# Optimization experiments

Hardware: AMD Instinct MI355X
Metric: run time of the kernel (lower is better)

The kernel has to match this reference:

```python
import jax, jax.numpy as jnp
import numpy as np
from jax import lax

NDF = 128
OUT_CH = 256
N_INPUT = 4096
H = W = 64
A_FEAT = OUT_CH * 2 * 2   # 1024
B_OUT = OUT_CH            # 256
C_ROW = 16
BATCH = 128
EPS = 1e-5


def conv2d_s2(x, w):
    # x: NCHW, w: OIHW, stride 2, pad 1 (kernel 4) -> halves spatial dims
    return lax.conv_general_dilated(x, w, window_strides=(2, 2),
                                    padding=[(1, 1), (1, 1)],
                                    dimension_numbers=("NCHW", "OIHW", "NCHW"))


def batchnorm(x, gamma, beta):
    # training-mode batch stats over (N, H, W)
    mean = jnp.mean(x, axis=(0, 2, 3), keepdims=True)
    var = jnp.var(x, axis=(0, 2, 3), keepdims=True)
    xn = (x - mean) * lax.rsqrt(var + EPS)
    return xn * gamma[None, :, None, None] + beta[None, :, None, None]


def lrelu(x):
    return jnp.where(x >= 0, x, 0.2 * x)


def setup_inputs() -> dict:
    key = jax.random.key(0)
    ks = jax.random.split(key, 16)
    s = lambda fan: 1.0 / np.sqrt(fan)
    inp = {
        "image": jax.random.normal(ks[0], (BATCH, 3, H, W), jnp.float32),
        "word_vectors": jax.random.normal(ks[1], (BATCH, N_INPUT), jnp.float32),
        "fc_w": jax.random.normal(ks[2], (H * W, N_INPUT), jnp.float32) * s(N_INPUT),
        "w1": jax.random.normal(ks[3], (NDF, 4, 4, 4), jnp.float32) * s(4 * 16),
        "w2": jax.random.normal(ks[4], (NDF * 2, NDF, 4, 4), jnp.float32) * s(NDF * 16),
        "w3": jax.random.normal(ks[5], (NDF * 2, NDF * 2, 4, 4), jnp.float32) * s(NDF * 2 * 16),
        "w4": jax.random.normal(ks[6], (NDF * 4, NDF * 2, 4, 4), jnp.float32) * s(NDF * 2 * 16),
        "w5": jax.random.normal(ks[7], (OUT_CH, NDF * 4, 4, 4), jnp.float32) * s(NDF * 4 * 16),
        "g2": jnp.ones((NDF * 2,), jnp.float32),
        "b2": jnp.zeros((NDF * 2,), jnp.float32),
        "g3": jnp.ones((NDF * 2,), jnp.float32),
        "b3": jnp.zeros((NDF * 2,), jnp.float32),
        "g4": jnp.ones((NDF * 4,), jnp.float32),
        "b4": jnp.zeros((NDF * 4,), jnp.float32),
        "T": jax.random.uniform(ks[8], (A_FEAT, B_OUT, C_ROW), jnp.float32,
                                 minval=0.0, maxval=1.0 / A_FEAT),
    }
    return inp


def reference(image, word_vectors, fc_w, w1, w2, w3, w4, w5,
              g2, b2, g3, b3, g4, b4, T):
    b = image.shape[0]
    # fc: Linear(no bias) + ReLU (dropout = identity at p=0 / eval)
    wv = jax.nn.relu(word_vectors @ fc_w.T)            # [b, H*W]
    wv = wv.reshape(b, 1, H, W)
    x = jnp.concatenate([image, wv], axis=1)           # [b, 4, 64, 64]
    # conv stack (spectral norm acts on weights; raw weights used here)
    x = lrelu(conv2d_s2(x, w1))                        # [b, ndf, 32, 32]
    x = lrelu(batchnorm(conv2d_s2(x, w2), g2, b2))     # [b, 2ndf, 16, 16]
    x = lrelu(batchnorm(conv2d_s2(x, w3), g3, b3))     # [b, 2ndf, 8, 8]
    x = lrelu(batchnorm(conv2d_s2(x, w4), g4, b4))     # [b, 4ndf, 4, 4]
    x = conv2d_s2(x, w5)                               # [b, out_ch, 2, 2]
    # minibatch discrimination
    feat = x.reshape(b, A_FEAT)                        # [b, 1024]
    Ms = (feat @ T.reshape(A_FEAT, B_OUT * C_ROW)).reshape(b, B_OUT, C_ROW)
    # pairwise L1 over C, exp, sum over batch (including self, as in the loop)
    d = jnp.sum(jnp.abs(Ms[:, None, :, :] - Ms[None, :, :, :]), axis=-1)  # [b,b,B]
    mbd = jnp.sum(jnp.exp(-d), axis=1)                 # [b, B]
    return jnp.concatenate([feat, mbd], axis=1)        # [b, 1280]
```

## Files before the change

kernel.cpp:

```cpp
#include <hip/hip_runtime.h>
#include <cstddef>

#define BB 128

typedef unsigned short u16;
typedef __attribute__((ext_vector_type(8))) short short8;
typedef __attribute__((ext_vector_type(4))) short short4v;
typedef __attribute__((ext_vector_type(4))) float f32x4;

constexpr int ilog2c(int v){ return v<=1 ? 0 : 1+ilog2c(v>>1); }

__device__ __forceinline__ u16 f2b(float f){
  union {float f; unsigned u;} x; x.f = f;
  unsigned u = x.u + 0x7fffu + ((x.u>>16)&1u);
  return (u16)(u>>16);
}
__device__ __forceinline__ float b2f(u16 h){
  union {unsigned u; float f;} x; x.u = ((unsigned)h)<<16;
  return x.f;
}

#define GLOAD_LDS16(gsrc, ldsdst) \
  __builtin_amdgcn_global_load_lds((const __attribute__((address_space(1))) void*)(gsrc), \
      (__attribute__((address_space(3))) void*)(ldsdst), 16, 0, 0)

template<int IC, int OC, int OH, int STORE, int KSPLIT=1>
__global__ __launch_bounds__(512) void convmm2(
    const u16* __restrict__ xp, const u16* __restrict__ wtT, void* __restrict__ yv)
{
  constexpr int OW = OH, S = OH*OW;
  constexpr int IHp = 2*OH+2, IWp = 2*OW+2;
  constexpr int KT = 16*IC;
  constexpr int KTS = KT / KSPLIT;
  constexpr int NT = KTS / 64;
  constexpr int M = BB * S;
  constexpr int LS = ilog2c(S), LOW = ilog2c(OW), L4 = ilog2c(4*IC);
  __shared__ u16 As[2*128*64];
  __shared__ u16 Bs[2*128*64];
  const int tid = threadIdx.x;
  const int n0 = blockIdx.x*128;
  const int m0 = blockIdx.y*128;
  const int kbase = (KSPLIT>1) ? blockIdx.z*KTS : 0;
  const int wave = tid>>6, l = tid&63;
  const int wm = wave>>1, wn = wave&1;

  size_t abase[2]; int au[2];
  #pragma unroll
  for (int t=0;t<2;++t){
    int unit = tid + t*512;
    int r = unit>>3, us = unit&7;
    au[t] = us ^ (r&7);
    int p = m0 + r;
    int b = p >> LS, s = p & (S-1);
    int oh = s >> LOW, ow = s & (OW-1);
    abase[t] = ((size_t)(b*IHp + 2*oh)*IWp + 2*ow)*IC;
  }
  const u16* bsrc[2];
  #pragma unroll
  for (int t=0;t<2;++t){
    int unit = tid + t*512;
    int r = unit>>3, us = unit&7;
    bsrc[t] = wtT + (size_t)(n0+r)*KT + (size_t)(us ^ (r&7))*8;
  }

  auto stage = [&](int half, int k0){
    #pragma unroll
    for (int t=0;t<2;++t){
      int k = k0 + au[t]*8;
      int kh = k >> L4, koff = k & (4*IC-1);
      GLOAD_LDS16(xp + abase[t] + (size_t)kh*IWp*IC + koff,
                  &As[half*8192 + (size_t)(t*512 + wave*64)*8]);
    }
    #pragma unroll
    for (int t=0;t<2;++t){
      GLOAD_LDS16(bsrc[t] + k0, &Bs[half*8192 + (size_t)(t*512 + wave*64)*8]);
    }
  };

  f32x4 acc[2][4] = {};

  stage(0, kbase);
  __syncthreads();
  int cur = 0;
  for (int t=0; t<NT; ++t){
    if (t+1 < NT) stage(cur^1, kbase + (t+1)*64);
    #pragma unroll
    for (int kk=0;kk<2;++kk){
      short8 af[2], bfm[4];
      #pragma unroll
      for (int mi=0;mi<2;++mi){
        int row = wm*32 + mi*16 + (l&15);
        int u = (kk*4 + (l>>4)) ^ (row&7);
        af[mi] = *(const short8*)(&As[cur*8192 + row*64 + u*8]);
      }
      #pragma unroll
      for (int ni=0;ni<4;++ni){
        int row = wn*64 + ni*16 + (l&15);
        int u = (kk*4 + (l>>4)) ^ (row&7);
        bfm[ni] = *(const short8*)(&Bs[cur*8192 + row*64 + u*8]);
      }
      #pragma unroll
      for (int mi=0;mi<2;++mi)
        #pragma unroll
        for (int ni=0;ni<4;++ni)
          acc[mi][ni] = __builtin_amdgcn_mfma_f32_16x16x32_bf16(af[mi], bfm[ni], acc[mi][ni], 0,0,0);
    }
    __syncthreads();
    cur ^= 1;
  }
  #pragma unroll
  for (int mi=0;mi<2;++mi){
    #pragma unroll
    for (int ni=0;ni<4;++ni){
      #pragma unroll
      for (int r=0;r<4;++r){
        int row = m0 + wm*32 + mi*16 + (l>>4)*4 + r;
        int col = n0 + wn*64 + ni*16 + (l&15);
        float v = acc[mi][ni][r];
        if (STORE==0){
          ((u16*)yv)[(size_t)row*OC + col] = f2b(v);
        } else if (STORE==1){
          v = v>=0.f ? v : 0.2f*v;
          int b = row>>LS, s = row&(S-1);
          int oh = s>>LOW, ow = s&(OW-1);
          ((u16*)yv)[((size_t)(b*(OH+2) + oh+1)*(OW+2) + ow+1)*OC + col] = f2b(v);
        } else {
          ((float*)yv)[((size_t)blockIdx.z*M + row)*OC + col] = v;
        }
      }
    }
  }
}

template<int B_FP32>
__global__ __launch_bounds__(256) void gemm128_split(
    const u16* __restrict__ A, const void* __restrict__ Bsrc,
    float* __restrict__ part, int K, int kchunk)
{
  __shared__ u16 As[2*128*64];
  __shared__ u16 Bs[2*64*64];
  const int tid = threadIdx.x;
  const int n0 = blockIdx.x*64;
  const int kbase = blockIdx.y*kchunk;
  const int wave = tid>>6, l = tid&63;
  const u16* asrc[4];
  #pragma unroll
  for (int t=0;t<4;++t){
    int unit = tid + t*256, r = unit>>3, us = unit&7;
    asrc[t] = A + (size_t)r*K + (size_t)(us ^ (r&7))*8;
  }
  const float* bf32[4]; int bdst32[4];
  const u16* b16[2];
  if (B_FP32){
    const float* Bf = (const float*)Bsrc;
    #pragma unroll
    for (int t=0;t<4;++t){
      int unit = tid + t*256;
      int r = unit>>4, u4 = unit&15;
      int u = u4>>1, hf = u4&1;
      int us = u ^ (r&7);
      bf32[t] = Bf + (size_t)(n0+r)*K + u4*4;
      bdst32[t] = r*64 + us*8 + hf*4;
    }
  } else {
    const u16* Bb = (const u16*)Bsrc;
    #pragma unroll
    for (int t=0;t<2;++t){
      int unit = tid + t*256, r = unit>>3, us = unit&7;
      b16[t] = Bb + (size_t)(n0+r)*K + (size_t)(us ^ (r&7))*8;
    }
  }

  auto stageA = [&](int half, int k0){
    #pragma unroll
    for (int t=0;t<4;++t)
      GLOAD_LDS16(asrc[t] + k0, &As[half*8192 + (size_t)(t*256 + wave*64)*8]);
  };
  auto stageB16 = [&](int half, int k0){
    #pragma unroll
    for (int t=0;t<2;++t)
      GLOAD_LDS16(b16[t] + k0, &Bs[half*4096 + (size_t)(t*256 + wave*64)*8]);
  };
  float4 breg[4];
  auto loadB32 = [&](int k0){
    #pragma unroll
    for (int t=0;t<4;++t) breg[t] = *(const float4*)(bf32[t] + k0);
  };
  auto writeB32 = [&](int half){
    #pragma unroll
    for (int t=0;t<4;++t){
      short4v o; o[0]=(short)f2b(breg[t].x); o[1]=(short)f2b(breg[t].y);
      o[2]=(short)f2b(breg[t].z); o[3]=(short)f2b(breg[t].w);
      *(short4v*)(&Bs[half*4096 + bdst32[t]]) = o;
    }
  };

  f32x4 acc[2][4] = {};
  const int NT = kchunk >> 6;
  stageA(0, kbase);
  if (B_FP32){ loadB32(kbase); writeB32(0); } else stageB16(0, kbase);
  __syncthreads();
  int cur = 0;
  for (int t=0;t<NT;++t){
    const int k0 = kbase + t*64;
    if (t+1 < NT){
      stageA(cur^1, k0+64);
      if (B_FP32) loadB32(k0+64);
      else stageB16(cur^1, k0+64);
    }
    #pragma unroll
    for (int kk=0;kk<2;++kk){
      short8 af[2], bfm[4];
      #pragma unroll
      for (int mi=0;mi<2;++mi){
        int row = wave*32 + mi*16 + (l&15);
        int u = (kk*4 + (l>>4)) ^ (row&7);
        af[mi] = *(const short8*)(&As[cur*8192 + row*64 + u*8]);
      }
      #pragma unroll
      for (int ni=0;ni<4;++ni){
        int row = ni*16 + (l&15);
        int u = (kk*4 + (l>>4)) ^ (row&7);
        bfm[ni] = *(const short8*)(&Bs[cur*4096 + row*64 + u*8]);
      }
      #pragma unroll
      for (int mi=0;mi<2;++mi)
        #pragma unroll
        for (int ni=0;ni<4;++ni)
          acc[mi][ni] = __builtin_amdgcn_mfma_f32_16x16x32_bf16(af[mi], bfm[ni], acc[mi][ni], 0,0,0);
    }
    if (B_FP32 && t+1 < NT) writeB32(cur^1);
    __syncthreads();
    cur ^= 1;
  }
  #pragma unroll
  for (int mi=0;mi<2;++mi){
    #pragma unroll
    for (int ni=0;ni<4;++ni){
      #pragma unroll
      for (int r=0;r<4;++r){
        int m = wave*32 + mi*16 + (l>>4)*4 + r;
        int n = n0 + ni*16 + (l&15);
        part[((size_t)blockIdx.y*128 + m)*4096 + n] = acc[mi][ni][r];
      }
    }
  }
}

template<int NS, int STORE>
__global__ __launch_bounds__(256) void reduce_split(const float* __restrict__ part, void* __restrict__ outv)
{
  int idx = blockIdx.x*256 + threadIdx.x;
  float s = 0.f;
  #pragma unroll
  for (int i=0;i<NS;++i) s += part[(size_t)i*524288 + idx];
  if (STORE==0){
    float v = fmaxf(s, 0.f);
    int m = idx>>12, n = idx&4095;
    int h = n>>6, w2 = n&63;
    ((u16*)outv)[((size_t)(m*66 + h+1)*66 + w2+1)*8 + 3] = f2b(v);
  } else {
    ((float*)outv)[idx] = s;
  }
}

template<int NS, int C>
__global__ __launch_bounds__(256) void reduce_bn(
    const float* __restrict__ part, u16* __restrict__ y,
    float* __restrict__ stats, int Mblk, int Mtot)
{
  constexpr int CU = C/8, NR = 256/CU, LCU = ilog2c(CU);
  __shared__ float red[NR*C];
  const int cu = threadIdx.x & (CU-1);
  const int rg = threadIdx.x >> LCU;
  const int base = blockIdx.x*Mblk;
  float s[8] = {}, ss[8] = {};
  for (int p = base+rg; p < base+Mblk; p += NR){
    float a8[8];
    #pragma unroll
    for (int j=0;j<8;++j) a8[j]=0.f;
    #pragma unroll
    for (int i=0;i<NS;++i){
      const float* src = part + ((size_t)i*Mtot + p)*C + cu*8;
      float4 v0 = *(const float4*)src;
      float4 v1 = *(const float4*)(src+4);
      a8[0]+=v0.x; a8[1]+=v0.y; a8[2]+=v0.z; a8[3]+=v0.w;
      a8[4]+=v1.x; a8[5]+=v1.y; a8[6]+=v1.z; a8[7]+=v1.w;
    }
    u16 o[8];
    #pragma unroll
    for (int j=0;j<8;++j){
      o[j] = f2b(a8[j]);
      float vb = b2f(o[j]);
      s[j]+=vb; ss[j]+=vb*vb;
    }
    *(short8*)(y + (size_t)p*C + cu*8) = *(short8*)o;
  }
  #pragma unroll
  for (int j=0;j<8;++j) red[rg*C + cu*8 + j] = s[j];
  __syncthreads();
  for (int c=threadIdx.x; c<C; c+=256){
    float t=0.f;
    #pragma unroll
    for (int r2=0;r2<NR;++r2) t += red[r2*C+c];
    stats[blockIdx.x*512 + c] = t;
  }
  __syncthreads();
  #pragma unroll
  for (int j=0;j<8;++j) red[rg*C + cu*8 + j] = ss[j];
  __syncthreads();
  for (int c=threadIdx.x; c<C; c+=256){
    float t=0.f;
    #pragma unroll
    for (int r2=0;r2<NR;++r2) t += red[r2*C+c];
    stats[131072 + blockIdx.x*512 + c] = t;
  }
}

__global__ __launch_bounds__(256) void conv5_reduce(const float* __restrict__ part,
                                                    float* __restrict__ out, u16* __restrict__ featb)
{
  int idx = blockIdx.x*256 + threadIdx.x;
  float s = 0.f;
  #pragma unroll
  for (int i=0;i<32;++i) s += part[(size_t)i*131072 + idx];
  int row = idx>>8, col = idx&255;
  int b = row>>2, sp = row&3;
  out[(size_t)b*1280 + col*4 + sp] = s;
  featb[(size_t)b*1024 + col*4 + sp] = f2b(s);
}

template<int IC, int ICP>
__device__ __forceinline__ void repack_dev(const float* __restrict__ w, u16* __restrict__ wt,
                                           int oc, int tid, float* ls){
  for (int i=tid; i<IC*16; i+=256){
    int ic = i>>4, khkw = i&15;
    ls[ic*17+khkw] = w[(size_t)oc*IC*16 + i];
  }
  __syncthreads();
  constexpr int KT = 16*ICP;
  constexpr int LP = ilog2c(ICP);
  for (int k=tid; k<KT; k+=256){
    int khkw = k >> LP, ic = k & (ICP-1);
    float v = (ic<IC) ? ls[ic*17+khkw] : 0.f;
    wt[(size_t)oc*KT + k] = f2b(v);
  }
}

__device__ __forceinline__ void transpose_dev(const float* __restrict__ T, u16* __restrict__ Tt,
                                              int idx, int tid, float* tile){
  int bx = idx & 127, by = idx >> 7;
  int kb = by*32, nb = bx*32;
  int tx = tid&31, ty = tid>>5;
  #pragma unroll
  for (int i=0;i<32;i+=8)
    tile[(ty+i)*33 + tx] = T[(size_t)(kb+ty+i)*4096 + nb+tx];
  __syncthreads();
  #pragma unroll
  for (int i=0;i<32;i+=8)
    Tt[(size_t)(nb+ty+i)*1024 + kb+tx] = f2b(tile[tx*33 + ty+i]);
}

__global__ __launch_bounds__(256) void prep_all(
    const float* __restrict__ w1, const float* __restrict__ w2, const float* __restrict__ w3,
    const float* __restrict__ w4, const float* __restrict__ w5, const float* __restrict__ T,
    const float* __restrict__ wvec,
    u16* wt1T, u16* wt2T, u16* wt3T, u16* wt4T, u16* wt5T, u16* Tt, u16* wvb)
{
  __shared__ float ls[512*17];
  const int blk = blockIdx.x, tid = threadIdx.x;
  if (blk < 128)        repack_dev<4,8>(w1, wt1T, blk, tid, ls);
  else if (blk < 384)   repack_dev<128,128>(w2, wt2T, blk-128, tid, ls);
  else if (blk < 640)   repack_dev<256,256>(w3, wt3T, blk-384, tid, ls);
  else if (blk < 1152)  repack_dev<256,256>(w4, wt4T, blk-640, tid, ls);
  else if (blk < 1408)  repack_dev<512,512>(w5, wt5T, blk-1152, tid, ls);
  else if (blk < 5504)  transpose_dev(T, Tt, blk-1408, tid, ls);
  else { int i = (blk-5504)*256 + tid; wvb[i] = f2b(wvec[i]); }
}

template<int Hp, int C>
__device__ __forceinline__ void zb_border(u16* __restrict__ buf, int idx, int count){
  if (idx >= count) return;
  constexpr int NP = 4*Hp - 4;
  constexpr int PC = NP*C;
  int b = idx / PC;
  int rem = idx - b*PC;
  int p = rem >> ilog2c(C);
  int c = rem & (C-1);
  int h, w;
  if (p < Hp){ h = 0; w = p; }
  else if (p < 2*Hp){ h = Hp-1; w = p - Hp; }
  else { int q = p - 2*Hp; h = 1 + (q>>1); w = (q&1) ? (Hp-1) : 0; }
  buf[(((size_t)b*Hp + h)*Hp + w)*C + c] = 0;
}

__global__ __launch_bounds__(256) void zb_early(u16* xp0, u16* xp1, u16* xp2){
  const int blk = blockIdx.x, tid = threadIdx.x;
  if (blk < 1040)       zb_border<66,8>(xp0, blk*256 + tid, 266240);
  else if (blk < 9488)  zb_border<34,128>(xp1, (blk-1040)*256 + tid, 2162688);
  else                  zb_border<18,256>(xp2, (blk-9488)*256 + tid, 2228224);
}

__global__ __launch_bounds__(256) void zb_late(u16* xp3, u16* xp4){
  const int blk = blockIdx.x, tid = threadIdx.x;
  if (blk < 4608) zb_border<10,256>(xp3, blk*256 + tid, 1179648);
  else            zb_border<6,512>(xp4, (blk-4608)*256 + tid, 1310720);
}

__global__ __launch_bounds__(256) void pack_x0(const float* __restrict__ img, u16* __restrict__ xp0){
  int idx = blockIdx.x*256+threadIdx.x;
  int b = idx>>12, s = idx&4095;
  int h = s>>6, w = s&63;
  short8 o = {};
  o[0] = (short)f2b(img[(size_t)(b*3+0)*4096 + s]);
  o[1] = (short)f2b(img[(size_t)(b*3+1)*4096 + s]);
  o[2] = (short)f2b(img[(size_t)(b*3+2)*4096 + s]);
  *(short8*)(xp0 + ((size_t)(b*66 + h+1)*66 + w+1)*8) = o;
}

template<int C>
__global__ __launch_bounds__(256) void bn_stats2(const u16* __restrict__ y, float* __restrict__ stats, int Mblk){
  constexpr int CU = C/8, NR = 256/CU, LCU = ilog2c(CU);
  __shared__ float red[NR*C];
  const int cu = threadIdx.x & (CU-1);
  const int rg = threadIdx.x >> LCU;
  const int base = blockIdx.x*Mblk;
  float s[8] = {}, ss[8] = {};
  for (int p = base+rg; p < base+Mblk; p += NR){
    short8 v = *(const short8*)(y + (size_t)p*C + cu*8);
    #pragma unroll
    for (int j=0;j<8;++j){ float f=b2f((u16)v[j]); s[j]+=f; ss[j]+=f*f; }
  }
  #pragma unroll
  for (int j=0;j<8;++j) red[rg*C + cu*8 + j] = s[j];
  __syncthreads();
  for (int c=threadIdx.x; c<C; c+=256){
    float t=0.f;
    #pragma unroll
    for (int r2=0;r2<NR;++r2) t += red[r2*C+c];
    stats[blockIdx.x*512 + c] = t;
  }
  __syncthreads();
  #pragma unroll
  for (int j=0;j<8;++j) red[rg*C + cu*8 + j] = ss[j];
  __syncthreads();
  for (int c=threadIdx.x; c<C; c+=256){
    float t=0.f;
    #pragma unroll
    for (int r2=0;r2<NR;++r2) t += red[r2*C+c];
    stats[131072 + blockIdx.x*512 + c] = t;
  }
}

template<int C>
__global__ __launch_bounds__(C) void bn_finalize(float* __restrict__ stats, const float* __restrict__ g,
                                                 const float* __restrict__ be, float cnt){
  int c = threadIdx.x;
  float s=0.f, ss=0.f;
  for (int b=0;b<256;++b){ s += stats[b*512+c]; ss += stats[131072 + b*512+c]; }
  float m = s/cnt;
  float var = ss/cnt - m*m;
  float A = rsqrtf(var + 1e-5f)*g[c];
  stats[262144 + c] = A;
  stats[262144 + 512 + c] = be[c] - m*A;
}

template<int C, int OH>
__global__ __launch_bounds__(256) void bn_apply(const u16* __restrict__ y, const float* __restrict__ stats,
                                                u16* __restrict__ xp){
  constexpr int S = OH*OH, LS = ilog2c(S), LOW = ilog2c(OH);
  constexpr int CU = C/8, LCU = ilog2c(CU);
  int idx = blockIdx.x*256 + threadIdx.x;
  int p = idx >> LCU, cu = idx & (CU-1);
  short8 v8 = *(const short8*)(y + (size_t)p*C + cu*8);
  const float* Ap = stats + 262144;
  const float* Bp = stats + 262144 + 512;
  u16 o[8];
  #pragma unroll
  for (int j=0;j<8;++j){
    float v = b2f((u16)v8[j])*Ap[cu*8+j] + Bp[cu*8+j];
    o[j] = f2b(v>=0.f ? v : 0.2f*v);
  }
  int b = p>>LS, s = p&(S-1), oh = s>>LOW, ow = s&(OH-1);
  *(short8*)(xp + ((size_t)(b*(OH+2)+oh+1)*(OH+2)+ow+1)*C + cu*8) = *(short8*)o;
}

__global__ __launch_bounds__(256) void mbd_kernel(
    const float* __restrict__ Ms, float* __restrict__ out)
{
  const int i = blockIdx.x;
  const int o = threadIdx.x;
  float mi[16];
  #pragma unroll
  for (int u = 0; u < 4; ++u) {
    float4 v = *(const float4*)&Ms[(size_t)i * 4096 + o * 16 + u * 4];
    mi[u*4+0]=v.x; mi[u*4+1]=v.y; mi[u*4+2]=v.z; mi[u*4+3]=v.w;
  }
  float acc = 0.f;
  for (int j = 0; j < BB; ++j) {
    float d = 0.f;
    #pragma unroll
    for (int u = 0; u < 4; ++u) {
      float4 v = *(const float4*)&Ms[(size_t)j * 4096 + o * 16 + u * 4];
      d += fabsf(mi[u*4+0]-v.x) + fabsf(mi[u*4+1]-v.y) + fabsf(mi[u*4+2]-v.z) + fabsf(mi[u*4+3]-v.w);
    }
    acc += __expf(-d);
  }
  out[(size_t)i * 1280 + 1024 + o] = acc;
}

__global__ void ws_too_small(float* out, int n){
  int idx = blockIdx.x*256+threadIdx.x;
  if (idx<n) out[idx] = -777.0f;
}

extern "C" void kernel_launch(void* const* d_in, const int* in_sizes, int n_in,
                              void* d_out, int out_size, void* d_ws, size_t ws_size,
                              hipStream_t stream)
{
  const float* image = (const float*)d_in[0];
  const float* wvec  = (const float*)d_in[1];
  const float* fc_w  = (const float*)d_in[2];
  const float* w1    = (const float*)d_in[3];
  const float* w2    = (const float*)d_in[4];
  const float* w3    = (const float*)d_in[5];
  const float* w4    = (const float*)d_in[6];
  const float* w5    = (const float*)d_in[7];
  const float* g2    = (const float*)d_in[8];
  const float* b2    = (const float*)d_in[9];
  const float* g3    = (const float*)d_in[10];
  const float* b3    = (const float*)d_in[11];
  const float* g4    = (const float*)d_in[12];
  const float* b4    = (const float*)d_in[13];
  const float* T     = (const float*)d_in[14];
  float* out = (float*)d_out;
  char* wsb = (char*)d_ws;

  const size_t NEED = 105816064ull;
  if (ws_size < NEED) {
    ws_too_small<<<(out_size + 255)/256, 256, 0, stream>>>(out, out_size);
    return;
  }

  u16* xp1   = (u16*)(wsb + 0);
  u16* y3    = (u16*)(wsb + 0);
  u16* xp3   = (u16*)(wsb + 4194304);
  u16* y4    = (u16*)(wsb + 10747904);
  u16* xp4   = (u16*)(wsb + 12845056);
  float* Ms  = (float*)(wsb + 17563648);
  u16* featb = (u16*)(wsb + 19660800);
  float* stats = (float*)(wsb + 19922944);
  u16* xp2   = (u16*)(wsb + 37879808);
  float* c4part = (float*)(wsb + 37879808);
  float* c5part = (float*)(wsb + 37879808);
  u16* y2    = (u16*)(wsb + 59113472);
  float* gpart  = (float*)(wsb + 59113472);
  float* c3part = (float*)(wsb + 59113472);
  u16* xp0   = (u16*)(wsb + 75890688);
  u16* wt1T  = (u16*)(wsb + 84811776);
  u16* wt2T  = (u16*)(wsb + 84844544);
  u16* wt3T  = (u16*)(wsb + 85893120);
  u16* wt4T  = (u16*)(wsb + 87990272);
  u16* wt5T  = (u16*)(wsb + 92184576);
  u16* Tt    = (u16*)(wsb + 96378880);
  u16* wvb   = (u16*)(wsb + 104767488);

  prep_all<<<7552, 256, 0, stream>>>(w1, w2, w3, w4, w5, T, wvec,
                                     wt1T, wt2T, wt3T, wt4T, wt5T, Tt, wvb);
  pack_x0<<<2048, 256, 0, stream>>>(image, xp0);
  zb_early<<<18192, 256, 0, stream>>>(xp0, xp1, xp2);

  gemm128_split<1><<<dim3(64,8), 256, 0, stream>>>(wvb, fc_w, gpart, 4096, 512);
  reduce_split<8,0><<<2048, 256, 0, stream>>>(gpart, xp0);

  convmm2<8,128,32,1><<<dim3(1,1024), 512, 0, stream>>>(xp0, wt1T, xp1);
  convmm2<128,256,16,0><<<dim3(2,256), 512, 0, stream>>>(xp1, wt2T, y2);

  zb_late<<<9728, 256, 0, stream>>>(xp3, xp4);

  bn_stats2<256><<<256, 256, 0, stream>>>(y2, stats, 128);
  bn_finalize<256><<<1, 256, 0, stream>>>(stats, g2, b2, 32768.f);
  bn_apply<256,16><<<4096, 256, 0, stream>>>(y2, stats, xp2);

  convmm2<256,256,8,3,2><<<dim3(2,64,2), 512, 0, stream>>>(xp2, wt3T, c3part);
  reduce_bn<2,256><<<256, 256, 0, stream>>>(c3part, y3, stats, 32, 8192);
  bn_finalize<256><<<1, 256, 0, stream>>>(stats, g3, b3, 8192.f);
  bn_apply<256,8><<<1024, 256, 0, stream>>>(y3, stats, xp3);

  convmm2<256,512,4,3,4><<<dim3(4,16,4), 512, 0, stream>>>(xp3, wt4T, c4part);
  reduce_bn<4,512><<<256, 256, 0, stream>>>(c4part, y4, stats, 8, 2048);
  bn_finalize<512><<<1, 512, 0, stream>>>(stats, g4, b4, 2048.f);
  bn_apply<512,4><<<512, 256, 0, stream>>>(y4, stats, xp4);

  convmm2<512,256,2,3,32><<<dim3(2,4,32), 512, 0, stream>>>(xp4, wt5T, c5part);
  conv5_reduce<<<512, 256, 0, stream>>>(c5part, out, featb);

  gemm128_split<0><<<dim3(64,8), 256, 0, stream>>>(featb, Tt, gpart, 1024, 128);
  reduce_split<8,1><<<2048, 256, 0, stream>>>(gpart, Ms);
  mbd_kernel<<<128, 256, 0, stream>>>(Ms, out);
}
```

Baseline: 288.8 us.

## Add triple-buffered conv GEMM kernel with configurable M tile for conv2-5

Introduces convmm3, a variant of the implicit-GEMM conv kernel that uses a three-stage LDS ring buffer with explicit vmcnt waits and a single barrier per k-step, prefetching two tiles ahead. It also sets MFMA priority around the compute. The M tile size is now a template parameter, and conv2 uses 256-row tiles (half the grid) to get more reuse of the weight tile per block. The goal is to hide global-to-LDS load latency and cut barrier overhead. The cost is more LDS per block, which can lower occupancy.

```diff
diff --git a/kernel.cpp b/kernel.cpp
--- a/kernel.cpp
+++ b/kernel.cpp
@@ -24,8 +24,14 @@
   __builtin_amdgcn_global_load_lds((const __attribute__((address_space(1))) void*)(gsrc), \
       (__attribute__((address_space(3))) void*)(ldsdst), 16, 0, 0)
 
-template<int IC, int OC, int OH, int STORE, int KSPLIT=1>
-__global__ __launch_bounds__(512) void convmm2(
+template<int N> __device__ __forceinline__ void vmwait(){
+  if constexpr (N==0)      asm volatile("s_waitcnt vmcnt(0)" ::: "memory");
+  else if constexpr (N==4) asm volatile("s_waitcnt vmcnt(4)" ::: "memory");
+  else if constexpr (N==6) asm volatile("s_waitcnt vmcnt(6)" ::: "memory");
+}
+
+template<int IC, int OC, int OH, int STORE, int KSPLIT, int BM>
+__global__ __launch_bounds__(512) void convmm3(
     const u16* __restrict__ xp, const u16* __restrict__ wtT, void* __restrict__ yv)
 {
   constexpr int OW = OH, S = OH*OW;
@@ -34,6 +40,122 @@
   constexpr int KTS = KT / KSPLIT;
   constexpr int NT = KTS / 64;
   constexpr int M = BB * S;
+  constexpr int LS = ilog2c(S), LOW = ilog2c(OW), L4 = ilog2c(4*IC);
+  constexpr int AU = BM/64;
+  constexpr int LL = AU + 2;
+  constexpr int FM = BM/64;
+  __shared__ u16 As[3*BM*64];
+  __shared__ u16 Bs[3*128*64];
+  const int tid = threadIdx.x;
+  const int n0 = blockIdx.x*128;
+  const int m0 = blockIdx.y*BM;
+  const int kbase = (KSPLIT>1) ? blockIdx.z*KTS : 0;
+  const int wave = tid>>6, l = tid&63;
+  const int wm = wave>>1, wn = wave&1;
+
+  size_t abase[AU]; int au[AU];
+  #pragma unroll
+  for (int t=0;t<AU;++t){
+    int unit = tid + t*512;
+    int r = unit>>3, us = unit&7;
+    au[t] = us ^ (r&7);
+    int p = m0 + r;
+    int b = p >> LS, s = p & (S-1);
+    int oh = s >> LOW, ow = s & (OW-1);
+    abase[t] = ((size_t)(b*IHp + 2*oh)*IWp + 2*ow)*IC;
+  }
+  const u16* bsrc[2];
+  #pragma unroll
+  for (int t=0;t<2;++t){
+    int unit = tid + t*512;
+    int r = unit>>3, us = unit&7;
+    bsrc[t] = wtT + (size_t)(n0+r)*KT + (size_t)(us ^ (r&7))*8;
+  }
+
+  auto stage = [&](int buf, int k0){
+    #pragma unroll
+    for (int t=0;t<AU;++t){
+      int k = k0 + au[t]*8;
+      int kh = k >> L4, koff = k & (4*IC-1);
+      GLOAD_LDS16(xp + abase[t] + (size_t)kh*IWp*IC + koff,
+                  &As[buf*BM*64 + (size_t)(t*512 + wave*64)*8]);
+    }
+    #pragma unroll
+    for (int t=0;t<2;++t){
+      GLOAD_LDS16(bsrc[t] + k0, &Bs[buf*8192 + (size_t)(t*512 + wave*64)*8]);
+    }
+  };
+
+  f32x4 acc[FM][4] = {};
+
+  stage(0, kbase);
+  stage(1, kbase + 64);
+  for (int t=0; t<NT; ++t){
+    const int buf = t - (t/3)*3;
+    if (t+1 < NT) vmwait<LL>(); else vmwait<0>();
+    __builtin_amdgcn_sched_barrier(0);
+    __builtin_amdgcn_s_barrier();
+    if (t+2 < NT){
+      int nb = (t+2) - ((t+2)/3)*3;
+      stage(nb, kbase + (t+2)*64);
+    }
+    #pragma unroll
+    for (int kk=0;kk<2;++kk){
+      short8 af[FM], bfm[4];
+      #pragma unroll
+      for (int mi=0;mi<FM;++mi){
+        int row = wm*(BM/4) + mi*16 + (l&15);
+        int u = (kk*4 + (l>>4)) ^ (row&7);
+        af[mi] = *(const short8*)(&As[buf*BM*64 + row*64 + u*8]);
+      }
+      #pragma unroll
+      for (int ni=0;ni<4;++ni){
+        int row = wn*64 + ni*16 + (l&15);
+        int u = (kk*4 + (l>>4)) ^ (row&7);
+        bfm[ni] = *(const short8*)(&Bs[buf*8192 + row*64 + u*8]);
+      }
+      __builtin_amdgcn_s_setprio(1);
+      #pragma unroll
+      for (int mi=0;mi<FM;++mi)
+        #pragma unroll
+        for (int ni=0;ni<4;++ni)
+          acc[mi][ni] = __builtin_amdgcn_mfma_f32_16x16x32_bf16(af[mi], bfm[ni], acc[mi][ni], 0,0,0);
+      __builtin_amdgcn_s_setprio(0);
+    }
+  }
+  #pragma unroll
+  for (int mi=0;mi<FM;++mi){
+    #pragma unroll
+    for (int ni=0;ni<4;++ni){
+      #pragma unroll
+      for (int r=0;r<4;++r){
+        int row = m0 + wm*(BM/4) + mi*16 + (l>>4)*4 + r;
+        int col = n0 + wn*64 + ni*16 + (l&15);
+        float v = acc[mi][ni][r];
+        if (STORE==0){
+          ((u16*)yv)[(size_t)row*OC + col] = f2b(v);
+        } else if (STORE==1){
+          v = v>=0.f ? v : 0.2f*v;
+          int b = row>>LS, s = row&(S-1);
+          int oh = s>>LOW, ow = s&(OW-1);
+          ((u16*)yv)[((size_t)(b*(OH+2) + oh+1)*(OW+2) + ow+1)*OC + col] = f2b(v);
+        } else {
+          ((float*)yv)[((size_t)blockIdx.z*M + row)*OC + col] = v;
+        }
+      }
+    }
+  }
+}
+
+template<int IC, int OC, int OH, int STORE, int KSPLIT=1>
+__global__ __launch_bounds__(512) void convmm2(
+    const u16* __restrict__ xp, const u16* __restrict__ wtT, void* __restrict__ yv)
+{
+  constexpr int OW = OH, S = OH*OW;
+  constexpr int IHp = 2*OH+2, IWp = 2*OW+2;
+  constexpr int KT = 16*IC;
+  constexpr int KTS = KT / KSPLIT;
+  constexpr int NT = KTS / 64;
   constexpr int LS = ilog2c(S), LOW = ilog2c(OW), L4 = ilog2c(4*IC);
   __shared__ u16 As[2*128*64];
   __shared__ u16 Bs[2*128*64];
@@ -125,7 +247,7 @@
           int oh = s>>LOW, ow = s&(OW-1);
           ((u16*)yv)[((size_t)(b*(OH+2) + oh+1)*(OW+2) + ow+1)*OC + col] = f2b(v);
         } else {
-          ((float*)yv)[((size_t)blockIdx.z*M + row)*OC + col] = v;
+          ((float*)yv)[((size_t)blockIdx.z*(BB*S) + row)*OC + col] = v;
         }
       }
     }
@@ -574,7 +696,7 @@
   reduce_split<8,0><<<2048, 256, 0, stream>>>(gpart, xp0);
 
   convmm2<8,128,32,1><<<dim3(1,1024), 512, 0, stream>>>(xp0, wt1T, xp1);
-  convmm2<128,256,16,0><<<dim3(2,256), 512, 0, stream>>>(xp1, wt2T, y2);
+  convmm3<128,256,16,0,1,256><<<dim3(2,128), 512, 0, stream>>>(xp1, wt2T, y2);
 
   zb_late<<<9728, 256, 0, stream>>>(xp3, xp4);
 
@@ -582,17 +704,17 @@
   bn_finalize<256><<<1, 256, 0, stream>>>(stats, g2, b2, 32768.f);
   bn_apply<256,16><<<4096, 256, 0, stream>>>(y2, stats, xp2);
 
-  convmm2<256,256,8,3,2><<<dim3(2,64,2), 512, 0, stream>>>(xp2, wt3T, c3part);
+  convmm3<256,256,8,3,2,128><<<dim3(2,64,2), 512, 0, stream>>>(xp2, wt3T, c3part);
   reduce_bn<2,256><<<256, 256, 0, stream>>>(c3part, y3, stats, 32, 8192);
   bn_finalize<256><<<1, 256, 0, stream>>>(stats, g3, b3, 8192.f);
   bn_apply<256,8><<<1024, 256, 0, stream>>>(y3, stats, xp3);
 
-  convmm2<256,512,4,3,4><<<dim3(4,16,4), 512, 0, stream>>>(xp3, wt4T, c4part);
+  convmm3<256,512,4,3,4,128><<<dim3(4,16,4), 512, 0, stream>>>(xp3, wt4T, c4part);
   reduce_bn<4,512><<<256, 256, 0, stream>>>(c4part, y4, stats, 8, 2048);
   bn_finalize<512><<<1, 512, 0, stream>>>(stats, g4, b4, 2048.f);
-  bn_apply<512,4><<<512, 256, 0, stream>>>(y4, stats, xp4);
-
-  convmm2<512,256,2,3,32><<<dim3(2,4,32), 512, 0, stream>>>(xp4, wt5T, c5part);
+  bn_apply<512,4><<<512, 0 ? 0 : 256, 0, stream>>>(y4, stats, xp4);
+
+  convmm3<512,256,2,3,32,128><<<dim3(2,4,32), 512, 0, stream>>>(xp4, wt5T, c5part);
   conv5_reduce<<<512, 256, 0, stream>>>(c5part, out, featb);
 
   gemm128_split<0><<<dim3(64,8), 256, 0, stream>>>(featb, Tt, gpart, 1024, 128);
```

Measured after the change: 302.3 us. 4.7% more time.
